# Optimization experiments

Measured on AMD Instinct MI355X. Metric: run time of the kernel, lower is better.

The kernel has to match this reference:

```python
import jax, jax.numpy as jnp
import numpy as np

B, S, D, O, E = 16, 512, 512, 512, 8


def setup_inputs() -> dict:
    key = jax.random.key(0)
    k1, k2, k3, k4, k5, k6 = jax.random.split(key, 6)
    x = jax.random.normal(k1, (B, S, D), dtype=jnp.float32)
    adj = jax.random.uniform(k2, (B, E, S, S), dtype=jnp.float32)
    # Stacked per-edge-type parameters (Gates: Linear(D,1); GraphConv: Linear(D,O))
    scale = 0.02
    Wg = jax.random.normal(k3, (E, D), dtype=jnp.float32) * scale  # gate weight, squeezed out-dim 1
    bg = jax.random.normal(k4, (E,), dtype=jnp.float32) * scale
    Wc = jax.random.normal(k5, (E, D, O), dtype=jnp.float32) * scale
    bc = jax.random.normal(k6, (E, O), dtype=jnp.float32) * scale
    return {"input": x, "adj": adj, "Wg": Wg, "bg": bg, "Wc": Wc, "bc": bc}


def reference(input, adj, Wg, bg, Wc, bc):
    # gate_status[e] = sigmoid(input @ Wg[e] + bg[e])  -> (B, E, S)
    gates = jax.nn.sigmoid(jnp.einsum('bsd,ed->bes', input, Wg) + bg[None, :, None])
    # h[e] = input @ Wc[e] + bc[e]                     -> (B, E, S, O)
    h = jnp.einsum('bsd,edo->beso', input, Wc) + bc[None, :, None, :]
    # adj_hat[e] = adj[:, e] * gates[e] broadcast over rows (gate of source node t)
    A = adj * gates[:, :, None, :]                     # (B, E, S, S)
    # sum over edge types of bmm(adj_hat, h), then relu
    out = jax.nn.relu(jnp.einsum('best,beto->bso', A, h))
    return out
```

## Files before the change

### kernel.cpp

```cpp
#include <hip/hip_runtime.h>
#include <stdint.h>

#define B_ 16
#define S_ 512
#define D_ 512
#define O_ 512
#define E_ 8

typedef unsigned short ushort_t;
typedef __attribute__((ext_vector_type(8))) short short8;
typedef __attribute__((ext_vector_type(8))) unsigned short ushort8;
typedef __attribute__((ext_vector_type(4))) unsigned short ushort4_t;
typedef __attribute__((ext_vector_type(4))) float f32x4;
typedef __attribute__((ext_vector_type(4))) unsigned int u32x4;

__device__ __forceinline__ ushort_t f2bf(float f) {
  union { float f; unsigned int u; } v; v.f = f;
  unsigned int u = v.u;
  return (ushort_t)((u + 0x7fffu + ((u >> 16) & 1u)) >> 16);
}

__device__ __forceinline__ float bf2f(ushort_t h) {
  union { unsigned int u; float f; } v; v.u = ((unsigned int)h) << 16;
  return v.f;
}

__device__ __forceinline__ unsigned int cvtpk(float lo, float hi) {
  unsigned int r;
  asm("v_cvt_pk_bf16_f32 %0, %1, %2" : "=v"(r) : "v"(lo), "v"(hi));
  return r;
}

__device__ __forceinline__ void gld_lds16(const void* g, void* l) {
  __builtin_amdgcn_global_load_lds((__attribute__((address_space(1))) void*)(g),
                                   (__attribute__((address_space(3))) void*)(l),
                                   16, 0, 0);
}


__global__ __launch_bounds__(256) void k_prep(const float* __restrict__ x,
                                              const float* __restrict__ Wg,
                                              const float* __restrict__ bg,
                                              float* __restrict__ gates,
                                              ushort_t* __restrict__ xb) {
  const int wave = threadIdx.x >> 6, lane = threadIdx.x & 63;
  const int row = blockIdx.x * 4 + wave;
  const float4* xr = (const float4*)(x + (size_t)row * D_);
  float4 x0 = xr[lane], x1 = xr[lane + 64];

  ushort4_t u0, u1;
  u0[0] = f2bf(x0.x); u0[1] = f2bf(x0.y); u0[2] = f2bf(x0.z); u0[3] = f2bf(x0.w);
  u1[0] = f2bf(x1.x); u1[1] = f2bf(x1.y); u1[2] = f2bf(x1.z); u1[3] = f2bf(x1.w);
  *(ushort4_t*)(xb + (size_t)row * D_ + 4 * lane) = u0;
  *(ushort4_t*)(xb + (size_t)row * D_ + 256 + 4 * lane) = u1;

  float p[E_];
#pragma unroll
  for (int e = 0; e < E_; ++e) {
    const float4* wr_ = (const float4*)(Wg + e * D_);
    float4 w0 = wr_[lane], w1 = wr_[lane + 64];
    p[e] = x0.x * w0.x + x0.y * w0.y + x0.z * w0.z + x0.w * w0.w +
           x1.x * w1.x + x1.y * w1.y + x1.z * w1.z + x1.w * w1.w;
  }
#pragma unroll
  for (int e = 0; e < E_; ++e) {
    float v = p[e];
#pragma unroll
    for (int off = 32; off > 0; off >>= 1) v += __shfl_xor(v, off, 64);
    p[e] = v;
  }
  const int b = row >> 9, s = row & (S_ - 1);
#pragma unroll
  for (int e = 0; e < E_; ++e)
    if (lane == e) {
      float z = p[e] + bg[e];
      gates[((size_t)(b * E_ + e)) * S_ + s] = 1.f / (1.f + __expf(-z));
    }
}

__global__ __launch_bounds__(256) void k_wcT(const float* __restrict__ Wc,
                                             ushort_t* __restrict__ WcT) {
  __shared__ float tile[64][65];
  const int e = blockIdx.z, d0 = blockIdx.y * 64, o0 = blockIdx.x * 64;
  const float* src = Wc + (size_t)e * D_ * O_;
#pragma unroll
  for (int i = 0; i < 16; ++i) {
    int idx = i * 256 + threadIdx.x;
    int r = idx >> 6, c = idx & 63;
    tile[r][c] = src[(size_t)(d0 + r) * O_ + o0 + c];
  }
  __syncthreads();
  ushort_t* dst = WcT + (size_t)e * O_ * D_;
#pragma unroll
  for (int i = 0; i < 16; ++i) {
    int idx = i * 256 + threadIdx.x;
    int r = idx >> 6, c = idx & 63;
    dst[(size_t)(o0 + r) * D_ + d0 + c] = f2bf(tile[c][r]);
  }
}


__global__ __launch_bounds__(256) void k_gemm1g(const ushort_t* __restrict__ WcT,
                                                const ushort_t* __restrict__ xb,
                                                const float* __restrict__ bc,
                                                const float* __restrict__ gates,
                                                ushort_t* __restrict__ hTg) {
  __shared__ __attribute__((aligned(16))) ushort_t lA[128 * 64];
  __shared__ __attribute__((aligned(16))) ushort_t lB[128 * 64];
  const int tid = threadIdx.x;
  const int m0 = blockIdx.x * 128, n0 = blockIdx.y * 128;
  const int tr = tid >> 3, tc = (tid & 7) * 8;
  const int lane = tid & 63, wid = tid >> 6;
  const int wr = wid >> 1, wc = wid & 1;
  const int lr = lane & 15, lk = (lane >> 4) * 8, lq = lane >> 4;

  f32x4 acc[4][4];
#pragma unroll
  for (int i = 0; i < 4; ++i)
#pragma unroll
    for (int j = 0; j < 4; ++j) acc[i][j] = (f32x4){0.f, 0.f, 0.f, 0.f};

  const ushort_t* gA = WcT + (size_t)(m0 + tr) * D_ + tc;
  const ushort_t* gB = xb + (size_t)(n0 + tr) * D_ + tc;

  for (int kk = 0; kk < 8; ++kk) {
    const int k0 = kk * 64;
    __syncthreads();
#pragma unroll
    for (int i = 0; i < 4; ++i) {
      gld_lds16(gA + (size_t)(32 * i) * D_ + k0, lA + tid * 8 + i * 2048);
      gld_lds16(gB + (size_t)(32 * i) * D_ + k0, lB + tid * 8 + i * 2048);
    }
    asm volatile("s_waitcnt vmcnt(0)" ::: "memory");
    __syncthreads();
    const ushort_t* pA = lA + (wr * 64 + lr) * 64 + lk;
    const ushort_t* pB = lB + (wc * 64 + lr) * 64 + lk;
#pragma unroll
    for (int ks = 0; ks < 2; ++ks) {
      short8 av[4], bv[4];
#pragma unroll
      for (int mi = 0; mi < 4; ++mi) av[mi] = *(const short8*)(pA + mi * 16 * 64 + ks * 32);
#pragma unroll
      for (int ni = 0; ni < 4; ++ni) bv[ni] = *(const short8*)(pB + ni * 16 * 64 + ks * 32);
#pragma unroll
      for (int mi = 0; mi < 4; ++mi)
#pragma unroll
        for (int ni = 0; ni < 4; ++ni)
          acc[mi][ni] = __builtin_amdgcn_mfma_f32_16x16x32_bf16(av[mi], bv[ni], acc[mi][ni], 0, 0, 0);
    }
  }

#pragma unroll
  for (int mi = 0; mi < 4; ++mi) {
    const int m_g = m0 + wr * 64 + mi * 16 + lq * 4;
    const int e = m_g >> 9;
#pragma unroll
    for (int ni = 0; ni < 4; ++ni) {
      const int n_g = n0 + wc * 64 + ni * 16 + lr;
      const int b = n_g >> 9, s = n_g & (S_ - 1);
      const float g = gates[((size_t)(b * E_ + e)) * S_ + s];
      f32x4 v = acc[mi][ni];
#pragma unroll
      for (int r = 0; r < 4; ++r)
        hTg[(size_t)(m_g + r) * (B_ * S_) + n_g] = f2bf((v[r] + bc[m_g + r]) * g);
    }
  }
}


#define LOAD_PFA(KIDX)                                                               \
  {                                                                                  \
    const int e_ = sp * EPB + ((KIDX) >> 3), t_ = ((KIDX) & 7) * 64;                 \
    const float* g_ = adj + ((size_t)((b * E_ + e_) * S_ + s0 + tr)) * S_ + t_ + tcf;\
    pf0 = *(const float4*)(g_);            pf1 = *(const float4*)(g_ + 4);           \
    pf2 = *(const float4*)(g_ + 32 * S_);  pf3 = *(const float4*)(g_ + 32 * S_ + 4); \
    pf4 = *(const float4*)(g_ + 64 * S_);  pf5 = *(const float4*)(g_ + 64 * S_ + 4); \
    pf6 = *(const float4*)(g_ + 96 * S_);  pf7 = *(const float4*)(g_ + 96 * S_ + 4); \
  }

#define ISSUE_B(BUF, KIDX)                                                           \
  {                                                                                  \
    const int e_ = sp * EPB + ((KIDX) >> 3), t_ = ((KIDX) & 7) * 64;                 \
    const ushort_t* g_ = hTg + ((size_t)(e_ * O_ + o0 + tr)) * (B_ * S_) +           \
                         b * S_ + t_ + chS * 8;                                      \
    gld_lds16(g_ + (size_t)0 * (B_ * S_),  &lB[BUF][tid * 8 + 0 * 2048]);            \
    gld_lds16(g_ + (size_t)32 * (B_ * S_), &lB[BUF][tid * 8 + 1 * 2048]);            \
    gld_lds16(g_ + (size_t)64 * (B_ * S_), &lB[BUF][tid * 8 + 2 * 2048]);            \
    gld_lds16(g_ + (size_t)96 * (B_ * S_), &lB[BUF][tid * 8 + 3 * 2048]);            \
  }

#define SUBITER(KK, RBUF, DOB, DOA, VM)                                              \
  {                                                                                  \
    __builtin_amdgcn_s_barrier();                                                    \
    __builtin_amdgcn_sched_barrier(0);                                               \
    if (DOB) ISSUE_B((RBUF) ^ 1, (KK) + 1);                                          \
    {                                    \
      u32x4 w_;                                                                      \
      w_[0] = cvtpk(pf0.x, pf0.y); w_[1] = cvtpk(pf0.z, pf0.w);                      \
      w_[2] = cvtpk(pf1.x, pf1.y); w_[3] = cvtpk(pf1.z, pf1.w);                      \
      *(u32x4*)(lA + 0 * 2048 + wrA) = w_;                                           \
      w_[0] = cvtpk(pf2.x, pf2.y); w_[1] = cvtpk(pf2.z, pf2.w);                      \
      w_[2] = cvtpk(pf3.x, pf3.y); w_[3] = cvtpk(pf3.z, pf3.w);                      \
      *(u32x4*)(lA + 1 * 2048 + wrA) = w_;                                           \
      w_[0] = cvtpk(pf4.x, pf4.y); w_[1] = cvtpk(pf4.z, pf4.w);                      \
      w_[2] = cvtpk(pf5.x, pf5.y); w_[3] = cvtpk(pf5.z, pf5.w);                      \
      *(u32x4*)(lA + 2 * 2048 + wrA) = w_;                                           \
      w_[0] = cvtpk(pf6.x, pf6.y); w_[1] = cvtpk(pf6.z, pf6.w);                      \
      w_[2] = cvtpk(pf7.x, pf7.y); w_[3] = cvtpk(pf7.z, pf7.w);                      \
      *(u32x4*)(lA + 3 * 2048 + wrA) = w_;                                           \
    }                                                                                \
    if (DOA) LOAD_PFA((KK) + 1);                                                     \
    asm volatile("s_waitcnt vmcnt(" #VM ") lgkmcnt(0)" ::: "memory");                \
    __builtin_amdgcn_sched_barrier(0);                                               \
    __builtin_amdgcn_s_barrier();                                                    \
    __builtin_amdgcn_sched_barrier(0);                                               \
    {                                                                                \
      const ushort_t* pA_ = lA + (wr * 64 + lr) * 64;                                \
      const ushort_t* pB_ = &lB[RBUF][(wc * 64 + lr) * 64];                          \
      __builtin_amdgcn_s_setprio(1);                                                 \
      _Pragma("unroll")                                                              \
      for (int ks = 0; ks < 2; ++ks) {                                               \
        const int co_ = ks ? cks1 : cks0;                                            \
        short8 av[4], bv[4];                                                         \
        _Pragma("unroll")                                                            \
        for (int mi = 0; mi < 4; ++mi) av[mi] = *(const short8*)(pA_ + mi * 1024 + co_);\
        _Pragma("unroll")                                                            \
        for (int ni = 0; ni < 4; ++ni) bv[ni] = *(const short8*)(pB_ + ni * 1024 + co_);\
        _Pragma("unroll")                                                            \
        for (int mi = 0; mi < 4; ++mi)                                               \
          _Pragma("unroll")                                                          \
          for (int ni = 0; ni < 4; ++ni)                                             \
            acc[mi][ni] = __builtin_amdgcn_mfma_f32_16x16x32_bf16(av[mi], bv[ni],    \
                                                                  acc[mi][ni], 0, 0, 0);\
      }                                                                              \
      __builtin_amdgcn_s_setprio(0);                                                 \
    }                                                                                \
  }

template <int SPLIT>
__global__ __launch_bounds__(256, 3) void k_gemm2f(const float* __restrict__ adj,
                                                   const ushort_t* __restrict__ hTg,
                                                   ushort_t* __restrict__ pdst,
                                                   float* __restrict__ fdst) {
  __shared__ __attribute__((aligned(16))) ushort_t lA[128 * 64];
  __shared__ __attribute__((aligned(16))) ushort_t lB[2][128 * 64];
  const int tid = threadIdx.x;
  const int w = blockIdx.x;
  const int xcd = w & 7;
  const int r_ = w >> 3;
  const int xo = r_ & 3;
  const int yo = (r_ >> 2) & 3;
  const int zhi = r_ >> 4;
  const int z = xcd + 8 * zhi;
  const int b = z / SPLIT, sp = z % SPLIT;
  const int o0 = xo * 128, s0 = yo * 128;
  constexpr int EPB = E_ / SPLIT;
  constexpr int NKK = EPB * 8;
  const int tr = tid >> 3;
  const int tcf = (tid & 7) * 8;
  const int chS = (tid & 7) ^ (tr & 7);
  const int wrA = tr * 64 + chS * 8;
  const int lane = tid & 63, wid = tid >> 6;
  const int wr = wid >> 1, wc = wid & 1;
  const int lr = lane & 15, lq = lane >> 4;
  const int rsw = lane & 7;
  const int cks0 = (((lane >> 4) + 0) ^ rsw) * 8;
  const int cks1 = (((lane >> 4) + 4) ^ rsw) * 8;

  f32x4 acc[4][4];
#pragma unroll
  for (int i = 0; i < 4; ++i)
#pragma unroll
    for (int j = 0; j < 4; ++j) acc[i][j] = (f32x4){0.f, 0.f, 0.f, 0.f};

  float4 pf0, pf1, pf2, pf3, pf4, pf5, pf6, pf7;

  LOAD_PFA(0);
  ISSUE_B(0, 0);

#pragma unroll 1
  for (int kk = 0; kk < NKK - 2; kk += 2) {
    SUBITER(kk, 0, 1, 1, 12)
    SUBITER(kk + 1, 1, 1, 1, 12)
  }
  SUBITER(NKK - 2, 0, 1, 1, 12)
  SUBITER(NKK - 1, 1, 0, 0, 0)

  if (SPLIT == 1) {
    float* base = fdst + (size_t)b * S_ * O_;
#pragma unroll
    for (int mi = 0; mi < 4; ++mi) {
      const int s_g = s0 + wr * 64 + mi * 16 + lq * 4;
#pragma unroll
      for (int ni = 0; ni < 4; ++ni) {
        const int o_g = o0 + wc * 64 + ni * 16 + lr;
        f32x4 v = acc[mi][ni];
#pragma unroll
        for (int r = 0; r < 4; ++r)
          base[(size_t)(s_g + r) * O_ + o_g] = fmaxf(v[r], 0.f);
      }
    }
  } else {
    ushort_t* base = pdst + ((size_t)sp * B_ + b) * S_ * O_;
#pragma unroll
    for (int mi = 0; mi < 4; ++mi) {
      const int s_g = s0 + wr * 64 + mi * 16 + lq * 4;
#pragma unroll
      for (int ni = 0; ni < 4; ++ni) {
        const int o_g = o0 + wc * 64 + ni * 16 + lr;
        f32x4 v = acc[mi][ni];
#pragma unroll
        for (int r = 0; r < 4; ++r)
          base[(size_t)(s_g + r) * O_ + o_g] = f2bf(v[r]);
      }
    }
  }
}

template <int SPLIT>
__global__ __launch_bounds__(256) void k_reduce(const ushort_t* __restrict__ part,
                                                float* __restrict__ out) {
  constexpr size_t N = (size_t)B_ * S_ * O_;
  size_t i8 = ((size_t)blockIdx.x * 256 + threadIdx.x) * 8;
  float a[8];
  ushort8 p0 = *(const ushort8*)(part + i8);
#pragma unroll
  for (int j = 0; j < 8; ++j) a[j] = bf2f(p0[j]);
#pragma unroll
  for (int s = 1; s < SPLIT; ++s) {
    ushort8 p = *(const ushort8*)(part + (size_t)s * N + i8);
#pragma unroll
    for (int j = 0; j < 8; ++j) a[j] += bf2f(p[j]);
  }
  f32x4 o0, o1;
  o0[0] = fmaxf(a[0], 0.f); o0[1] = fmaxf(a[1], 0.f);
  o0[2] = fmaxf(a[2], 0.f); o0[3] = fmaxf(a[3], 0.f);
  o1[0] = fmaxf(a[4], 0.f); o1[1] = fmaxf(a[5], 0.f);
  o1[2] = fmaxf(a[6], 0.f); o1[3] = fmaxf(a[7], 0.f);
  *(f32x4*)(out + i8) = o0;
  *(f32x4*)(out + i8 + 4) = o1;
}


extern "C" void kernel_launch(void* const* d_in, const int* in_sizes, int n_in,
                              void* d_out, int out_size, void* d_ws, size_t ws_size,
                              hipStream_t stream) {
  const float* x   = (const float*)d_in[0];
  const float* adj = (const float*)d_in[1];
  const float* Wg  = (const float*)d_in[2];
  const float* bg  = (const float*)d_in[3];
  const float* Wc  = (const float*)d_in[4];
  const float* bc  = (const float*)d_in[5];
  float* out = (float*)d_out;

  char* ws = (char*)d_ws;
  float* gates  = (float*)ws;    ws += (size_t)B_ * E_ * S_ * 4;
  ushort_t* xb  = (ushort_t*)ws; ws += (size_t)B_ * S_ * D_ * 2;
  ushort_t* WcT = (ushort_t*)ws; ws += (size_t)E_ * O_ * D_ * 2;
  ushort_t* hTg = (ushort_t*)ws; ws += (size_t)E_ * O_ * B_ * S_ * 2;
  ushort_t* part = (ushort_t*)ws;
  const size_t base_bytes = (size_t)((char*)part - (char*)d_ws);
  const size_t part_sz = (size_t)B_ * S_ * O_ * sizeof(ushort_t);

  int split = 1;
  if (ws_size >= base_bytes + 4 * part_sz) split = 4;
  else if (ws_size >= base_bytes + 2 * part_sz) split = 2;

  k_prep<<<dim3((B_ * S_) / 4), dim3(256), 0, stream>>>(x, Wg, bg, gates, xb);
  k_wcT<<<dim3(O_ / 64, D_ / 64, E_), dim3(256), 0, stream>>>(Wc, WcT);
  k_gemm1g<<<dim3((E_ * O_) / 128, (B_ * S_) / 128), dim3(256), 0, stream>>>(WcT, xb, bc, gates, hTg);

  const int red_blocks = (int)(((size_t)B_ * S_ * O_) / (256 * 8));
  if (split == 4) {
    k_gemm2f<4><<<dim3(16 * B_ * 4), dim3(256), 0, stream>>>(adj, hTg, part, nullptr);
    k_reduce<4><<<dim3(red_blocks), dim3(256), 0, stream>>>(part, out);
  } else if (split == 2) {
    k_gemm2f<2><<<dim3(16 * B_ * 2), dim3(256), 0, stream>>>(adj, hTg, part, nullptr);
    k_reduce<2><<<dim3(red_blocks), dim3(256), 0, stream>>>(part, out);
  } else {
    k_gemm2f<1><<<dim3(16 * B_), dim3(256), 0, stream>>>(adj, hTg, nullptr, out);
  }
}
```

Baseline: 147.5 us.

## Use 512-thread blocks in aggregation GEMM with smaller per-wave tiles

Doubles the aggregation GEMM block to 8 waves, each computing a 32x64 subtile instead of 64x64, and splits the global load and LDS staging work across all 512 threads. The goal is more waves in flight to hide global-load latency and cut per-thread register pressure. The wait before the second barrier now covers only LDS counters, with no explicit wait on outstanding global loads. Per-wave MFMA work halves while barrier cost is shared by more waves.

```diff
diff --git a/kernel.cpp b/kernel.cpp
--- a/kernel.cpp
+++ b/kernel.cpp
@@ -171,63 +171,52 @@
 #define LOAD_PFA(KIDX)                                                               \
   {                                                                                  \
     const int e_ = sp * EPB + ((KIDX) >> 3), t_ = ((KIDX) & 7) * 64;                 \
-    const float* g_ = adj + ((size_t)((b * E_ + e_) * S_ + s0 + tr)) * S_ + t_ + tcf;\
-    pf0 = *(const float4*)(g_);            pf1 = *(const float4*)(g_ + 4);           \
-    pf2 = *(const float4*)(g_ + 32 * S_);  pf3 = *(const float4*)(g_ + 32 * S_ + 4); \
-    pf4 = *(const float4*)(g_ + 64 * S_);  pf5 = *(const float4*)(g_ + 64 * S_ + 4); \
-    pf6 = *(const float4*)(g_ + 96 * S_);  pf7 = *(const float4*)(g_ + 96 * S_ + 4); \
+    const float* g_ = adj + ((size_t)((b * E_ + e_) * S_ + s0 + rA)) * S_ + t_ + qA * 16;\
+    pf0 = *(const float4*)(g_);      pf1 = *(const float4*)(g_ + 4);                 \
+    pf2 = *(const float4*)(g_ + 8);  pf3 = *(const float4*)(g_ + 12);                \
   }
 
 #define ISSUE_B(BUF, KIDX)                                                           \
   {                                                                                  \
     const int e_ = sp * EPB + ((KIDX) >> 3), t_ = ((KIDX) & 7) * 64;                 \
-    const ushort_t* g_ = hTg + ((size_t)(e_ * O_ + o0 + tr)) * (B_ * S_) +           \
-                         b * S_ + t_ + chS * 8;                                      \
-    gld_lds16(g_ + (size_t)0 * (B_ * S_),  &lB[BUF][tid * 8 + 0 * 2048]);            \
-    gld_lds16(g_ + (size_t)32 * (B_ * S_), &lB[BUF][tid * 8 + 1 * 2048]);            \
-    gld_lds16(g_ + (size_t)64 * (B_ * S_), &lB[BUF][tid * 8 + 2 * 2048]);            \
-    gld_lds16(g_ + (size_t)96 * (B_ * S_), &lB[BUF][tid * 8 + 3 * 2048]);            \
-  }
-
-#define SUBITER(KK, RBUF, DOB, DOA, VM)                                              \
+    const ushort_t* gb_ = hTg + (size_t)(e_ * O_ + o0) * (B_ * S_) + b * S_ + t_ + chSrc * 8;\
+    gld_lds16(gb_ + (size_t)rB0 * (B_ * S_), &lB[BUF][wv * 1024 + 0 * 512 + l8]);    \
+    gld_lds16(gb_ + (size_t)rB1 * (B_ * S_), &lB[BUF][wv * 1024 + 1 * 512 + l8]);    \
+  }
+
+#define SUBITER(KK, RBUF, DOB, DOA)                                                  \
   {                                                                                  \
     __builtin_amdgcn_s_barrier();                                                    \
     __builtin_amdgcn_sched_barrier(0);                                               \
     if (DOB) ISSUE_B((RBUF) ^ 1, (KK) + 1);                                          \
-    {                                    \
+    {                                   \
       u32x4 w_;                                                                      \
       w_[0] = cvtpk(pf0.x, pf0.y); w_[1] = cvtpk(pf0.z, pf0.w);                      \
       w_[2] = cvtpk(pf1.x, pf1.y); w_[3] = cvtpk(pf1.z, pf1.w);                      \
-      *(u32x4*)(lA + 0 * 2048 + wrA) = w_;                                           \
+      *(u32x4*)(lA + wrA0) = w_;                                                     \
       w_[0] = cvtpk(pf2.x, pf2.y); w_[1] = cvtpk(pf2.z, pf2.w);                      \
       w_[2] = cvtpk(pf3.x, pf3.y); w_[3] = cvtpk(pf3.z, pf3.w);                      \
-      *(u32x4*)(lA + 1 * 2048 + wrA) = w_;                                           \
-      w_[0] = cvtpk(pf4.x, pf4.y); w_[1] = cvtpk(pf4.z, pf4.w);                      \
-      w_[2] = cvtpk(pf5.x, pf5.y); w_[3] = cvtpk(pf5.z, pf5.w);                      \
-      *(u32x4*)(lA + 2 * 2048 + wrA) = w_;                                           \
-      w_[0] = cvtpk(pf6.x, pf6.y); w_[1] = cvtpk(pf6.z, pf6.w);                      \
-      w_[2] = cvtpk(pf7.x, pf7.y); w_[3] = cvtpk(pf7.z, pf7.w);                      \
-      *(u32x4*)(lA + 3 * 2048 + wrA) = w_;                                           \
+      *(u32x4*)(lA + wrA1) = w_;                                                     \
     }                                                                                \
     if (DOA) LOAD_PFA((KK) + 1);                                                     \
-    asm volatile("s_waitcnt vmcnt(" #VM ") lgkmcnt(0)" ::: "memory");                \
+    asm volatile("s_waitcnt lgkmcnt(0)" ::: "memory");                               \
     __builtin_amdgcn_sched_barrier(0);                                               \
     __builtin_amdgcn_s_barrier();                                                    \
     __builtin_amdgcn_sched_barrier(0);                                               \
     {                                                                                \
-      const ushort_t* pA_ = lA + (wr * 64 + lr) * 64;                                \
-      const ushort_t* pB_ = &lB[RBUF][(wc * 64 + lr) * 64];                          \
+      const ushort_t* pA_ = lA + (wrow * 32 + lr) * 64;                              \
+      const ushort_t* pB_ = &lB[RBUF][(wcol * 64 + lr) * 64];                        \
       __builtin_amdgcn_s_setprio(1);                                                 \
       _Pragma("unroll")                                                              \
       for (int ks = 0; ks < 2; ++ks) {                                               \
         const int co_ = ks ? cks1 : cks0;                                            \
-        short8 av[4], bv[4];                                                         \
+        short8 av[2], bv[4];                                                         \
         _Pragma("unroll")                                                            \
-        for (int mi = 0; mi < 4; ++mi) av[mi] = *(const short8*)(pA_ + mi * 1024 + co_);\
+        for (int mi = 0; mi < 2; ++mi) av[mi] = *(const short8*)(pA_ + mi * 1024 + co_);\
         _Pragma("unroll")                                                            \
         for (int ni = 0; ni < 4; ++ni) bv[ni] = *(const short8*)(pB_ + ni * 1024 + co_);\
         _Pragma("unroll")                                                            \
-        for (int mi = 0; mi < 4; ++mi)                                               \
+        for (int mi = 0; mi < 2; ++mi)                                               \
           _Pragma("unroll")                                                          \
           for (int ni = 0; ni < 4; ++ni)                                             \
             acc[mi][ni] = __builtin_amdgcn_mfma_f32_16x16x32_bf16(av[mi], bv[ni],    \
@@ -238,7 +227,7 @@
   }
 
 template <int SPLIT>
-__global__ __launch_bounds__(256, 3) void k_gemm2f(const float* __restrict__ adj,
+__global__ __launch_bounds__(512, 6) void k_gemm2f(const float* __restrict__ adj,
                                                    const ushort_t* __restrict__ hTg,
                                                    ushort_t* __restrict__ pdst,
                                                    float* __restrict__ fdst) {
@@ -256,44 +245,47 @@
   const int o0 = xo * 128, s0 = yo * 128;
   constexpr int EPB = E_ / SPLIT;
   constexpr int NKK = EPB * 8;
-  const int tr = tid >> 3;
-  const int tcf = (tid & 7) * 8;
-  const int chS = (tid & 7) ^ (tr & 7);
-  const int wrA = tr * 64 + chS * 8;
+
+  const int rA = tid >> 2, qA = tid & 3;
+  const int wrA0 = rA * 64 + (((qA * 2 + 0) ^ (rA & 7)) * 8);
+  const int wrA1 = rA * 64 + (((qA * 2 + 1) ^ (rA & 7)) * 8);
+  const int wv = tid >> 6, l = tid & 63;
+  const int rB0 = wv * 16 + (l >> 3), rB1 = wv * 16 + (l >> 3) + 8;
+  const int chSrc = (l & 7) ^ ((l >> 3) & 7);
+  const int l8 = l * 8;
   const int lane = tid & 63, wid = tid >> 6;
-  const int wr = wid >> 1, wc = wid & 1;
+  const int wrow = wid >> 1, wcol = wid & 1;
   const int lr = lane & 15, lq = lane >> 4;
-  const int rsw = lane & 7;
-  const int cks0 = (((lane >> 4) + 0) ^ rsw) * 8;
-  const int cks1 = (((lane >> 4) + 4) ^ rsw) * 8;
-
-  f32x4 acc[4][4];
-#pragma unroll
-  for (int i = 0; i < 4; ++i)
+  const int cks0 = (((lane >> 4) + 0) ^ (lane & 7)) * 8;
+  const int cks1 = (((lane >> 4) + 4) ^ (lane & 7)) * 8;
+
+  f32x4 acc[2][4];
+#pragma unroll
+  for (int i = 0; i < 2; ++i)
 #pragma unroll
     for (int j = 0; j < 4; ++j) acc[i][j] = (f32x4){0.f, 0.f, 0.f, 0.f};
 
-  float4 pf0, pf1, pf2, pf3, pf4, pf5, pf6, pf7;
-
+  float4 pf0, pf1, pf2, pf3;
+
+  ISSUE_B(0, 0);
   LOAD_PFA(0);
-  ISSUE_B(0, 0);
 
 #pragma unroll 1
   for (int kk = 0; kk < NKK - 2; kk += 2) {
-    SUBITER(kk, 0, 1, 1, 12)
-    SUBITER(kk + 1, 1, 1, 1, 12)
-  }
-  SUBITER(NKK - 2, 0, 1, 1, 12)
-  SUBITER(NKK - 1, 1, 0, 0, 0)
+    SUBITER(kk, 0, 1, 1)
+    SUBITER(kk + 1, 1, 1, 1)
+  }
+  SUBITER(NKK - 2, 0, 1, 1)
+  SUBITER(NKK - 1, 1, 0, 0)
 
   if (SPLIT == 1) {
     float* base = fdst + (size_t)b * S_ * O_;
 #pragma unroll
-    for (int mi = 0; mi < 4; ++mi) {
-      const int s_g = s0 + wr * 64 + mi * 16 + lq * 4;
+    for (int mi = 0; mi < 2; ++mi) {
+      const int s_g = s0 + wrow * 32 + mi * 16 + lq * 4;
 #pragma unroll
       for (int ni = 0; ni < 4; ++ni) {
-        const int o_g = o0 + wc * 64 + ni * 16 + lr;
+        const int o_g = o0 + wcol * 64 + ni * 16 + lr;
         f32x4 v = acc[mi][ni];
 #pragma unroll
         for (int r = 0; r < 4; ++r)
@@ -303,11 +295,11 @@
   } else {
     ushort_t* base = pdst + ((size_t)sp * B_ + b) * S_ * O_;
 #pragma unroll
-    for (int mi = 0; mi < 4; ++mi) {
-      const int s_g = s0 + wr * 64 + mi * 16 + lq * 4;
+    for (int mi = 0; mi < 2; ++mi) {
+      const int s_g = s0 + wrow * 32 + mi * 16 + lq * 4;
 #pragma unroll
       for (int ni = 0; ni < 4; ++ni) {
-        const int o_g = o0 + wc * 64 + ni * 16 + lr;
+        const int o_g = o0 + wcol * 64 + ni * 16 + lr;
         f32x4 v = acc[mi][ni];
 #pragma unroll
         for (int r = 0; r < 4; ++r)
@@ -372,12 +364,12 @@
 
   const int red_blocks = (int)(((size_t)B_ * S_ * O_) / (256 * 8));
   if (split == 4) {
-    k_gemm2f<4><<<dim3(16 * B_ * 4), dim3(256), 0, stream>>>(adj, hTg, part, nullptr);
+    k_gemm2f<4><<<dim3(16 * B_ * 4), dim3(512), 0, stream>>>(adj, hTg, part, nullptr);
     k_reduce<4><<<dim3(red_blocks), dim3(256), 0, stream>>>(part, out);
   } else if (split == 2) {
-    k_gemm2f<2><<<dim3(16 * B_ * 2), dim3(256), 0, stream>>>(adj, hTg, part, nullptr);
+    k_gemm2f<2><<<dim3(16 * B_ * 2), dim3(512), 0, stream>>>(adj, hTg, part, nullptr);
     k_reduce<2><<<dim3(red_blocks), dim3(256), 0, stream>>>(part, out);
   } else {
-    k_gemm2f<1><<<dim3(16 * B_), dim3(256), 0, stream>>>(adj, hTg, nullptr, out);
-  }
-}
+    k_gemm2f<1><<<dim3(16 * B_), dim3(512), 0, stream>>>(adj, hTg, nullptr, out);
+  }
+}
```

After: 254.7 us. 1.73x slower.
